# Optimization experiments

Hardware: AMD Instinct MI355X
Metric: run time of the kernel (lower is better)

Reference implementation:

```python
import jax, jax.numpy as jnp
import numpy as np

N = 50000      # nodes per graph
E = 800000     # edges per graph
F_IN = 128     # num_node_features
HID = 128      # hidden_dim
OUT = 128      # output_dim
C = 40         # num_classes
NEG_SLOPE = 0.2


def setup_inputs() -> dict:
    key = jax.random.key(0)
    ks = jax.random.split(key, 28)
    def p(k, shape, scale=0.05):
        return jax.random.normal(k, shape, jnp.float32) * scale
    inp = {
        "x": jax.random.normal(ks[0], (N, F_IN), jnp.float32),
        "y": jax.random.normal(ks[1], (N, F_IN), jnp.float32),
        "edge_index_x": jax.random.randint(ks[2], (2, E), 0, N),
        "edge_index_y": jax.random.randint(ks[3], (2, E), 0, N),
        # MultiheadAttention 1 (packed qkv in_proj like torch)
        "attn1_in_w": p(ks[4], (3 * F_IN, F_IN)),
        "attn1_in_b": p(ks[5], (3 * F_IN,)),
        "attn1_out_w": p(ks[6], (F_IN, F_IN)),
        "attn1_out_b": p(ks[7], (F_IN,)),
        # MultiheadAttention 2
        "attn2_in_w": p(ks[8], (3 * F_IN, F_IN)),
        "attn2_in_b": p(ks[9], (3 * F_IN,)),
        "attn2_out_w": p(ks[10], (F_IN, F_IN)),
        "attn2_out_b": p(ks[11], (F_IN,)),
        # gat1 (shared by x and y paths)
        "gat1_w": p(ks[12], (HID, F_IN)),
        "gat1_asrc": p(ks[13], (HID,)),
        "gat1_adst": p(ks[14], (HID,)),
        "gat1_b": p(ks[15], (HID,)),
        # gat2_x
        "gat2x_w": p(ks[16], (OUT, HID)),
        "gat2x_asrc": p(ks[17], (OUT,)),
        "gat2x_adst": p(ks[18], (OUT,)),
        "gat2x_b": p(ks[19], (OUT,)),
        # gat2_y
        "gat2y_w": p(ks[20], (OUT, HID)),
        "gat2y_asrc": p(ks[21], (OUT,)),
        "gat2y_adst": p(ks[22], (OUT,)),
        "gat2y_b": p(ks[23], (OUT,)),
        # fc
        "fc_w": p(ks[24], (C, 2 * OUT + F_IN)),
        "fc_b": p(ks[25], (C,)),
    }
    return inp


def _mha_len1(x, in_w, in_b, out_w, out_b):
    # x.unsqueeze(0) in torch -> seq_len=1 (batch=N). Softmax over a single
    # key is identically 1, so attention output == V; q/k projections cancel.
    d = x.shape[-1]
    v = x @ in_w[2 * d:].T + in_b[2 * d:]
    return v @ out_w.T + out_b


def _gat_conv(x, edge_index, W, a_src, a_dst, b):
    # PyG GATConv, heads=1, concat=True, add_self_loops=True
    n = x.shape[0]
    loop = jnp.arange(n)
    src = jnp.concatenate([edge_index[0], loop])  # message sources j
    dst = jnp.concatenate([edge_index[1], loop])  # message targets i
    h = x @ W.T                                   # [n, out]
    e = jax.nn.leaky_relu((h @ a_src)[src] + (h @ a_dst)[dst], NEG_SLOPE)
    # segment softmax over destination node neighborhoods
    m = jax.ops.segment_max(e, dst, num_segments=n)
    ex = jnp.exp(e - m[dst])
    s = jax.ops.segment_sum(ex, dst, num_segments=n)
    alpha = ex / (s[dst] + 1e-16)
    out = jax.ops.segment_sum(alpha[:, None] * h[src], dst, num_segments=n)
    return out + b


def reference(x, y, edge_index_x, edge_index_y,
              attn1_in_w, attn1_in_b, attn1_out_w, attn1_out_b,
              attn2_in_w, attn2_in_b, attn2_out_w, attn2_out_b,
              gat1_w, gat1_asrc, gat1_adst, gat1_b,
              gat2x_w, gat2x_asrc, gat2x_adst, gat2x_b,
              gat2y_w, gat2y_asrc, gat2y_adst, gat2y_b,
              fc_w, fc_b):
    x_res = x
    xa = _mha_len1(x, attn1_in_w, attn1_in_b, attn1_out_w, attn1_out_b)
    hx = jax.nn.relu(_gat_conv(xa, edge_index_x, gat1_w, gat1_asrc, gat1_adst, gat1_b))
    # dropout is a no-op in eval mode
    ox = _gat_conv(hx, edge_index_x, gat2x_w, gat2x_asrc, gat2x_adst, gat2x_b)

    ya = _mha_len1(y, attn2_in_w, attn2_in_b, attn2_out_w, attn2_out_b)
    hy = jax.nn.relu(_gat_conv(ya, edge_index_y, gat1_w, gat1_asrc, gat1_adst, gat1_b))
    oy = _gat_conv(hy, edge_index_y, gat2y_w, gat2y_asrc, gat2y_adst, gat2y_b)

    fusion = jnp.concatenate([ox, oy, x_res], axis=1)
    out = fusion @ fc_w.T + fc_b
    return jax.nn.log_softmax(out, axis=1)
```

## Files before the change

### kernel.cpp

```cpp
#include <hip/hip_runtime.h>
#include <hip/hip_bf16.h>
#include <hip/hip_fp16.h>

#define NEG_SLOPE 0.2f
#define LOG_R 10
#define RPB (1 << LOG_R)
#define EPB 4096
#define CAPB 24576

typedef __attribute__((ext_vector_type(4))) float f32x4;
typedef __attribute__((ext_vector_type(2))) float f32x2;
typedef __attribute__((ext_vector_type(8))) short s16x8;

static __device__ __forceinline__ unsigned pkbf(float a, float b) {
    unsigned ua = __float_as_uint(a);
    ua = (ua + 0x7FFFu + ((ua >> 16) & 1u)) >> 16;
    unsigned ub = __float_as_uint(b);
    ub = (ub + 0x7FFFu + ((ub >> 16) & 1u)) & 0xFFFF0000u;
    return (ua & 0xFFFFu) | ub;
}
static __device__ __forceinline__ unsigned short bf1(float a) {
    unsigned ua = __float_as_uint(a);
    return (unsigned short)((ua + 0x7FFFu + ((ua >> 16) & 1u)) >> 16);
}
static __device__ __forceinline__ float bflo(unsigned u) { return __uint_as_float(u << 16); }
static __device__ __forceinline__ float bfhi(unsigned u) { return __uint_as_float(u & 0xFFFF0000u); }

__global__ __launch_bounds__(256) void mha_combine2(
    const float* __restrict__ iw1, const float* __restrict__ ib1,
    const float* __restrict__ ow1, const float* __restrict__ ob1,
    const float* __restrict__ iw2, const float* __restrict__ ib2,
    const float* __restrict__ ow2, const float* __restrict__ ob2,
    float* __restrict__ cw1, float* __restrict__ cb1,
    float* __restrict__ cw2, float* __restrict__ cb2)
{
    int idx = blockIdx.x * blockDim.x + threadIdx.x;
    int set = idx >> 14;
    int local = idx & 16383;
    int o = local >> 7, i = local & 127;
    const float* in_w  = set ? iw2 : iw1;
    const float* in_b  = set ? ib2 : ib1;
    const float* out_w = set ? ow2 : ow1;
    const float* out_b = set ? ob2 : ob1;
    float* combW = set ? cw2 : cw1;
    float* combb = set ? cb2 : cb1;
    float a = 0.f;
    for (int k = 0; k < 128; ++k)
        a = fmaf(out_w[o * 128 + k], in_w[(256 + k) * 128 + i], a);
    combW[local] = a;
    if (i == 0) {
        float b = out_b[o];
        for (int k = 0; k < 128; ++k)
            b = fmaf(out_w[o * 128 + k], in_b[256 + k], b);
        combb[o] = b;
    }
}

template<bool ABF, bool HFP8>
__global__ __launch_bounds__(256) void gemm_mfma2(
    const void* __restrict__ A0, const void* __restrict__ A1,
    const float* __restrict__ W0, const float* __restrict__ W1,
    const float* __restrict__ bias0, const float* __restrict__ bias1,
    const float* __restrict__ as0, const float* __restrict__ ad0,
    const float* __restrict__ as1, const float* __restrict__ ad1,
    void* __restrict__ h0, void* __restrict__ h1,
    float* __restrict__ ss0, float* __restrict__ sd0,
    float* __restrict__ ss1, float* __restrict__ sd1,
    int n, int half)
{
    __shared__ unsigned xl[64 * 64];
    __shared__ unsigned wl[128 * 64];

    int b = blockIdx.x;
    const void* Ain; const float *W, *bias, *asrc, *adst;
    void* hbs; float *ssrc, *sdst;
    if (b < half) { Ain = A0; W = W0; bias = bias0; asrc = as0; adst = ad0; hbs = h0; ssrc = ss0; sdst = sd0; }
    else { b -= half; Ain = A1; W = W1; bias = bias1; asrc = as1; adst = ad1; hbs = h1; ssrc = ss1; sdst = sd1; }

    const int t = threadIdx.x;
    const int row0 = b * 64;

#pragma unroll
    for (int i = 0; i < 4; ++i) {
        int q = t + i * 256;
        int r = q >> 4, sl = q & 15;
        int gr = row0 + r; if (gr >= n) gr = n - 1;
        unsigned p0, p1, p2, p3;
        if (ABF) {
            uint4 v = ((const uint4*)Ain)[(size_t)gr * 16 + sl];
            p0 = v.x; p1 = v.y; p2 = v.z; p3 = v.w;
        } else {
            float4 a = ((const float4*)Ain)[(size_t)gr * 32 + sl * 2];
            float4 bb = ((const float4*)Ain)[(size_t)gr * 32 + sl * 2 + 1];
            p0 = pkbf(a.x, a.y); p1 = pkbf(a.z, a.w);
            p2 = pkbf(bb.x, bb.y); p3 = pkbf(bb.z, bb.w);
        }
        int dsl = sl ^ (r & 7);
        *(uint4*)&xl[r * 64 + dsl * 4] = make_uint4(p0, p1, p2, p3);
    }
#pragma unroll
    for (int i = 0; i < 8; ++i) {
        int q = t + i * 256;
        int r = q >> 4, sl = q & 15;
        float4 a = ((const float4*)W)[(size_t)r * 32 + sl * 2];
        float4 bb = ((const float4*)W)[(size_t)r * 32 + sl * 2 + 1];
        int dsl = sl ^ (r & 7);
        *(uint4*)&wl[r * 64 + dsl * 4] = make_uint4(
            pkbf(a.x, a.y), pkbf(a.z, a.w), pkbf(bb.x, bb.y), pkbf(bb.z, bb.w));
    }
    __syncthreads();

    const int l = t & 63, w = t >> 6;
    const int c = l & 15, q4 = l >> 4;
    const int rloc = w * 16 + c;
    f32x4 acc[8];
#pragma unroll
    for (int nt = 0; nt < 8; ++nt) acc[nt] = (f32x4){0.f, 0.f, 0.f, 0.f};

#pragma unroll
    for (int s = 0; s < 4; ++s) {
        int slot = (s * 4 + q4) ^ (c & 7);
        s16x8 af = *(const s16x8*)&xl[rloc * 64 + slot * 4];
#pragma unroll
        for (int nt = 0; nt < 8; ++nt) {
            int wr = nt * 16 + c;
            s16x8 bfr = *(const s16x8*)&wl[wr * 64 + slot * 4];
            acc[nt] = __builtin_amdgcn_mfma_f32_16x16x32_bf16(af, bfr, acc[nt], 0, 0, 0);
        }
    }

    float bv[8], as8[8], ad8[8];
#pragma unroll
    for (int nt = 0; nt < 8; ++nt) {
        bv[nt]  = bias ? bias[nt * 16 + c] : 0.f;
        as8[nt] = asrc ? asrc[nt * 16 + c] : 0.f;
        ad8[nt] = asrc ? adst[nt * 16 + c] : 0.f;
    }
    float ps[4] = {0.f, 0.f, 0.f, 0.f}, pd[4] = {0.f, 0.f, 0.f, 0.f};
    const int grow0 = row0 + w * 16 + q4 * 4;
#pragma unroll
    for (int nt = 0; nt < 8; ++nt) {
#pragma unroll
        for (int j = 0; j < 4; ++j) {
            float val = acc[nt][j] + bv[nt];
            if (grow0 + j < n) {
                if (HFP8) {
                    unsigned b8 = (unsigned)__builtin_amdgcn_cvt_pk_fp8_f32(val, val, 0, false);
                    ((unsigned char*)hbs)[(size_t)(grow0 + j) * 128 + nt * 16 + c] = (unsigned char)b8;
                } else {
                    ((unsigned short*)hbs)[(size_t)(grow0 + j) * 128 + nt * 16 + c] = bf1(val);
                }
            }
            ps[j] = fmaf(val, as8[nt], ps[j]);
            pd[j] = fmaf(val, ad8[nt], pd[j]);
        }
    }
    if (asrc) {
#pragma unroll
        for (int j = 0; j < 4; ++j) {
            float a = ps[j], bb = pd[j];
#pragma unroll
            for (int o = 1; o < 16; o <<= 1) {
                a += __shfl_xor(a, o);
                bb += __shfl_xor(bb, o);
            }
            if (c == 0 && grow0 + j < n) { ssrc[grow0 + j] = a; sdst[grow0 + j] = bb; }
        }
    }
}


__global__ __launch_bounds__(256) void hist_bucket2(
    const int* __restrict__ eix, const int* __restrict__ eiy, int E, int n,
    int* __restrict__ bcx, int* __restrict__ bcy, int half)
{
    __shared__ int lh[64];
    int gb = blockIdx.x;
    const int* ei = eix; int* bc = bcx;
    if (gb >= half) { gb -= half; ei = eiy; bc = bcy; }
    int t = threadIdx.x;
    int ET = E + n;
    int nbk = (n + RPB - 1) >> LOG_R;
    for (int i = t; i < nbk; i += 256) lh[i] = 0;
    __syncthreads();
    for (int e = gb * 256 + t; e < ET; e += half * 256) {
        int d = (e < E) ? ei[E + e] : (e - E);
        atomicAdd(&lh[d >> LOG_R], 1);
    }
    __syncthreads();
    if (t < nbk) atomicAdd(&bc[t], lh[t]);
}

__global__ void bscan(
    const int* __restrict__ bcx, const int* __restrict__ bcy, int nbk,
    int* __restrict__ bbx, int* __restrict__ bby,
    int* __restrict__ curx, int* __restrict__ cury,
    int* __restrict__ offx_n, int* __restrict__ offy_n)
{
    int w = threadIdx.x >> 6, lane = threadIdx.x & 63;
    if (w > 1) return;
    const int* bc = w ? bcy : bcx;
    int* bb  = w ? bby : bbx;
    int* cur = w ? cury : curx;
    int* offn = w ? offy_n : offx_n;
    int c = (lane < nbk) ? bc[lane] : 0;
    int v = c;
#pragma unroll
    for (int o = 1; o < 64; o <<= 1) {
        int u = __shfl_up(v, o);
        if (lane >= o) v += u;
    }
    int excl = v - c;
    if (lane < nbk) { bb[lane] = excl; cur[lane] = excl; }
    if (lane == 63) { bb[nbk] = v; *offn = v; }
}

__global__ __launch_bounds__(256) void bucket_pass(
    const int* __restrict__ eix, const int* __restrict__ eiy, int E, int n,
    int* __restrict__ curx, int* __restrict__ cury,
    unsigned* __restrict__ pkx, unsigned* __restrict__ pky, int half)
{
    __shared__ int lhist[64], lbase[64], gbase[64], lpos[64];
    __shared__ unsigned stg[EPB];
    __shared__ int gidx[EPB];
    int gb = blockIdx.x;
    const int* ei = eix; int* bcur = curx; unsigned* pk = pkx;
    if (gb >= half) { gb -= half; ei = eiy; bcur = cury; pk = pky; }
    const int t = threadIdx.x;
    const int ET = E + n;
    const int nbk = (n + RPB - 1) >> LOG_R;
    const int base = gb * EPB;

    for (int i = t; i < nbk; i += 256) lhist[i] = 0;
    __syncthreads();

    unsigned mypk[16];
    int myb[16];
#pragma unroll
    for (int k = 0; k < 16; ++k) {
        int e = base + k * 256 + t;
        if (e < ET) {
            int s, d;
            if (e < E) { s = ei[e]; d = ei[E + e]; }
            else       { s = e - E; d = e - E; }
            myb[k] = d >> LOG_R;
            mypk[k] = ((unsigned)s << LOG_R) | (unsigned)(d & (RPB - 1));
            atomicAdd(&lhist[myb[k]], 1);
        } else myb[k] = -1;
    }
    __syncthreads();

    if (t < 64) {
        int c = (t < nbk) ? lhist[t] : 0;
        int v = c;
#pragma unroll
        for (int o = 1; o < 64; o <<= 1) {
            int u = __shfl_up(v, o);
            if (t >= o) v += u;
        }
        int excl = v - c;
        if (t < nbk) {
            lbase[t] = excl;
            lpos[t] = excl;
            gbase[t] = c ? atomicAdd(&bcur[t], c) : 0;
        }
    }
    __syncthreads();

#pragma unroll
    for (int k = 0; k < 16; ++k) {
        if (myb[k] >= 0) {
            int p = atomicAdd(&lpos[myb[k]], 1);
            stg[p] = mypk[k];
            gidx[p] = gbase[myb[k]] + (p - lbase[myb[k]]);
        }
    }
    __syncthreads();

    int tot = lbase[nbk - 1] + lhist[nbk - 1];
    for (int i = t; i < tot; i += 256) pk[gidx[i]] = stg[i];
}

__global__ __launch_bounds__(256) void fine_sort(
    const unsigned* __restrict__ pkx, const unsigned* __restrict__ pky,
    const int* __restrict__ bbx, const int* __restrict__ bby,
    int* __restrict__ offx, int* __restrict__ offy,
    unsigned short* __restrict__ csx, unsigned short* __restrict__ csy,
    int n, int half)
{
    __shared__ int cur[RPB];
    __shared__ int ws[256];
    __shared__ unsigned short outs[CAPB];
    int gb = blockIdx.x;
    const unsigned* pk; const int* bb; int* off; unsigned short* cs;
    if (gb < half) { pk = pkx; bb = bbx; off = offx; cs = csx; }
    else { gb -= half; pk = pky; bb = bby; off = offy; cs = csy; }
    const int t = threadIdx.x;
    const int d0 = gb << LOG_R;
    const int nd = min(RPB, n - d0);
    const int base = bb[gb];
    const int sz = bb[gb + 1] - base;

    for (int i = t; i < RPB; i += 256) cur[i] = 0;
    __syncthreads();
    for (int i = t; i < sz; i += 256)
        atomicAdd(&cur[pk[base + i] & (RPB - 1)], 1);
    __syncthreads();

    int c0 = cur[t * 4], c1 = cur[t * 4 + 1], c2 = cur[t * 4 + 2], c3 = cur[t * 4 + 3];
    int s = c0 + c1 + c2 + c3;
    ws[t] = s; __syncthreads();
    for (int o = 1; o < 256; o <<= 1) {
        int a = (t >= o) ? ws[t - o] : 0;
        __syncthreads();
        ws[t] += a;
        __syncthreads();
    }
    int ex = ws[t] - s;
    int e0 = ex, e1 = ex + c0, e2 = e1 + c1, e3 = e2 + c2;
    cur[t * 4] = e0; cur[t * 4 + 1] = e1; cur[t * 4 + 2] = e2; cur[t * 4 + 3] = e3;
    int i0 = t * 4;
    if (i0     < nd) off[d0 + i0]     = base + e0;
    if (i0 + 1 < nd) off[d0 + i0 + 1] = base + e1;
    if (i0 + 2 < nd) off[d0 + i0 + 2] = base + e2;
    if (i0 + 3 < nd) off[d0 + i0 + 3] = base + e3;
    __syncthreads();

    if (sz <= CAPB) {
        for (int i = t; i < sz; i += 256) {
            unsigned p = pk[base + i];
            int pos = atomicAdd(&cur[p & (RPB - 1)], 1);
            outs[pos] = (unsigned short)(p >> LOG_R);
        }
        __syncthreads();
        for (int i = t; i < sz; i += 256) cs[base + i] = outs[i];
    } else {
        for (int i = t; i < sz; i += 256) {
            unsigned p = pk[base + i];
            int pos = atomicAdd(&cur[p & (RPB - 1)], 1);
            cs[base + pos] = (unsigned short)(p >> LOG_R);
        }
    }
}

__global__ __launch_bounds__(256) void gat_aggregate2(
    const int* __restrict__ off0, const unsigned short* __restrict__ cs0,
    const float* __restrict__ ss0, const float* __restrict__ sd0,
    const unsigned char* __restrict__ hb0, const float* __restrict__ bias0,
    unsigned* __restrict__ out0,
    const int* __restrict__ off1, const unsigned short* __restrict__ cs1,
    const float* __restrict__ ss1, const float* __restrict__ sd1,
    const unsigned char* __restrict__ hb1, const float* __restrict__ bias1,
    unsigned* __restrict__ out1,
    int n, int relu, int half)
{
    __shared__ uint2 stg[4][2][32];
    int b = blockIdx.x;
    const int *off; const unsigned short *csrc; const float *ssrc, *sdst, *bias;
    const unsigned char* hb; unsigned* outu;
    if (b < half) { off = off0; csrc = cs0; ssrc = ss0; sdst = sd0; hb = hb0; bias = bias0; outu = out0; }
    else { b -= half; off = off1; csrc = cs1; ssrc = ss1; sdst = sd1; hb = hb1; bias = bias1; outu = out1; }

    const int w = threadIdx.x >> 6;
    const int lane = threadIdx.x & 63;
    const int hw = lane >> 5;
    const int l32 = lane & 31;
    int node = b * 8 + w * 2 + hw;
    const int valid = node < n;
    if (node >= n) node = n - 1;
    const int p0 = off[node], p1 = off[node + 1];
    const int deg = p1 - p0;
    const float sd = sdst[node];

    unsigned mysrc = 0; float myv = -INFINITY;
    if (l32 < deg) {
        mysrc = csrc[p0 + l32];
        float v = ssrc[mysrc] + sd;
        myv = (v > 0.f) ? v : NEG_SLOPE * v;
    }
    float m = myv;
    for (int p = p0 + 32 + l32; p < p1; p += 32) {
        int s = csrc[p];
        float v = ssrc[s] + sd;
        v = (v > 0.f) ? v : NEG_SLOPE * v;
        m = fmaxf(m, v);
    }
#pragma unroll
    for (int o = 16; o; o >>= 1) m = fmaxf(m, __shfl_xor(m, o));

    float myex = (l32 < deg) ? __expf(myv - m) : 0.f;
    float part = myex;
    for (int p = p0 + 32 + l32; p < p1; p += 32) {
        int s = csrc[p];
        float v = ssrc[s] + sd;
        v = (v > 0.f) ? v : NEG_SLOPE * v;
        part += __expf(v - m);
    }
    float ssum = part;
#pragma unroll
    for (int o = 16; o; o >>= 1) ssum += __shfl_xor(ssum, o);

    stg[w][hw][l32] = make_uint2(mysrc, __float_as_uint(myex));

    const unsigned clo = (unsigned)l32 * 4u;
    float a0 = 0.f, a1 = 0.f, a2 = 0.f, a3 = 0.f;

    int jcap = deg < 32 ? deg : 32;
    int j = 0;
    for (; j + 8 <= jcap; j += 8) {
        uint2 q[8];
#pragma unroll
        for (int k = 0; k < 8; ++k) q[k] = stg[w][hw][j + k];
        unsigned u[8];
#pragma unroll
        for (int k = 0; k < 8; ++k)
            u[k] = *(const unsigned*)(hb + (((size_t)q[k].x << 7) | clo));
#pragma unroll
        for (int k = 0; k < 8; ++k) {
            f32x2 flo = __builtin_amdgcn_cvt_pk_f32_fp8((int)u[k], false);
            f32x2 fhi = __builtin_amdgcn_cvt_pk_f32_fp8((int)u[k], true);
            float e = __uint_as_float(q[k].y);
            a0 = fmaf(e, flo[0], a0);
            a1 = fmaf(e, flo[1], a1);
            a2 = fmaf(e, fhi[0], a2);
            a3 = fmaf(e, fhi[1], a3);
        }
    }
    for (; j < jcap; ++j) {
        uint2 q = stg[w][hw][j];
        unsigned u = *(const unsigned*)(hb + (((size_t)q.x << 7) | clo));
        f32x2 flo = __builtin_amdgcn_cvt_pk_f32_fp8((int)u, false);
        f32x2 fhi = __builtin_amdgcn_cvt_pk_f32_fp8((int)u, true);
        float e = __uint_as_float(q.y);
        a0 = fmaf(e, flo[0], a0);
        a1 = fmaf(e, flo[1], a1);
        a2 = fmaf(e, fhi[0], a2);
        a3 = fmaf(e, fhi[1], a3);
    }
    for (int p = p0 + 32; p < p1; ++p) {
        int s = csrc[p];
        float v = ssrc[s] + sd;
        v = (v > 0.f) ? v : NEG_SLOPE * v;
        float e = __expf(v - m);
        unsigned u = *(const unsigned*)(hb + (((size_t)s << 7) | clo));
        f32x2 flo = __builtin_amdgcn_cvt_pk_f32_fp8((int)u, false);
        f32x2 fhi = __builtin_amdgcn_cvt_pk_f32_fp8((int)u, true);
        a0 = fmaf(e, flo[0], a0);
        a1 = fmaf(e, flo[1], a1);
        a2 = fmaf(e, fhi[0], a2);
        a3 = fmaf(e, fhi[1], a3);
    }

    float inv = 1.f / (ssum + 1e-16f);
    float4 bv = ((const float4*)bias)[l32];
    float o0 = fmaf(a0, inv, bv.x);
    float o1 = fmaf(a1, inv, bv.y);
    float o2 = fmaf(a2, inv, bv.z);
    float o3 = fmaf(a3, inv, bv.w);
    if (relu) {
        o0 = fmaxf(o0, 0.f); o1 = fmaxf(o1, 0.f);
        o2 = fmaxf(o2, 0.f); o3 = fmaxf(o3, 0.f);
    }
    if (valid)
        ((uint2*)(outu + (size_t)node * 64))[l32] = make_uint2(pkbf(o0, o1), pkbf(o2, o3));
}

__global__ __launch_bounds__(256) void fc_logsoftmax(
    const unsigned* __restrict__ oxu, const unsigned* __restrict__ oyu,
    const float* __restrict__ xres,
    const float* __restrict__ fcw, const float* __restrict__ fcb,
    float* __restrict__ out, int n)
{
    __shared__ float wt[40 * 132];
    const int t = threadIdx.x;
    const int node0 = blockIdx.x * 128;
    const int c0 = (t & 7) * 5;
    int gr[4];
#pragma unroll
    for (int j = 0; j < 4; ++j) {
        gr[j] = node0 + (t >> 3) * 4 + j;
        if (gr[j] >= n) gr[j] = n - 1;
    }

    float acc[4][5] = {};

    for (int kc = 0; kc < 3; ++kc) {
        __syncthreads();
        for (int i = t; i < 40 * 32; i += 256) {
            int cc = i >> 5, c4 = i & 31;
            *(float4*)&wt[cc * 132 + c4 * 4] = ((const float4*)fcw)[(size_t)cc * 96 + kc * 32 + c4];
        }
        __syncthreads();
#pragma unroll 4
        for (int k4 = 0; k4 < 32; ++k4) {
            float4 xv[4];
            if (kc == 2) {
#pragma unroll
                for (int j = 0; j < 4; ++j)
                    xv[j] = ((const float4*)xres)[(size_t)gr[j] * 32 + k4];
            } else {
                const unsigned* S = kc ? oyu : oxu;
#pragma unroll
                for (int j = 0; j < 4; ++j) {
                    uint2 u = *(const uint2*)&S[(size_t)gr[j] * 64 + k4 * 2];
                    xv[j] = make_float4(bflo(u.x), bfhi(u.x), bflo(u.y), bfhi(u.y));
                }
            }
#pragma unroll
            for (int j5 = 0; j5 < 5; ++j5) {
                float4 wv = *(const float4*)&wt[(c0 + j5) * 132 + k4 * 4];
#pragma unroll
                for (int j = 0; j < 4; ++j) {
                    acc[j][j5] = fmaf(xv[j].x, wv.x, acc[j][j5]);
                    acc[j][j5] = fmaf(xv[j].y, wv.y, acc[j][j5]);
                    acc[j][j5] = fmaf(xv[j].z, wv.z, acc[j][j5]);
                    acc[j][j5] = fmaf(xv[j].w, wv.w, acc[j][j5]);
                }
            }
        }
    }

    float fb[5];
#pragma unroll
    for (int j5 = 0; j5 < 5; ++j5) fb[j5] = fcb[c0 + j5];

#pragma unroll
    for (int j = 0; j < 4; ++j) {
        float m0 = -INFINITY;
#pragma unroll
        for (int j5 = 0; j5 < 5; ++j5) { acc[j][j5] += fb[j5]; m0 = fmaxf(m0, acc[j][j5]); }
#pragma unroll
        for (int o = 1; o < 8; o <<= 1) m0 = fmaxf(m0, __shfl_xor(m0, o));
        float s0 = 0.f;
#pragma unroll
        for (int j5 = 0; j5 < 5; ++j5) s0 += __expf(acc[j][j5] - m0);
#pragma unroll
        for (int o = 1; o < 8; o <<= 1) s0 += __shfl_xor(s0, o);
        float lse = m0 + logf(s0);
#pragma unroll
        for (int j5 = 0; j5 < 5; ++j5)
            out[(size_t)gr[j] * 40 + c0 + j5] = acc[j][j5] - lse;
    }
}

extern "C" void kernel_launch(void* const* d_in, const int* in_sizes, int n_in,
                              void* d_out, int out_size, void* d_ws, size_t ws_size,
                              hipStream_t stream)
{
    const float* x    = (const float*)d_in[0];
    const float* y    = (const float*)d_in[1];
    const int*   eix  = (const int*)d_in[2];
    const int*   eiy  = (const int*)d_in[3];
    const float* a1iw = (const float*)d_in[4];
    const float* a1ib = (const float*)d_in[5];
    const float* a1ow = (const float*)d_in[6];
    const float* a1ob = (const float*)d_in[7];
    const float* a2iw = (const float*)d_in[8];
    const float* a2ib = (const float*)d_in[9];
    const float* a2ow = (const float*)d_in[10];
    const float* a2ob = (const float*)d_in[11];
    const float* g1w  = (const float*)d_in[12];
    const float* g1as = (const float*)d_in[13];
    const float* g1ad = (const float*)d_in[14];
    const float* g1b  = (const float*)d_in[15];
    const float* g2xw = (const float*)d_in[16];
    const float* g2xas= (const float*)d_in[17];
    const float* g2xad= (const float*)d_in[18];
    const float* g2xb = (const float*)d_in[19];
    const float* g2yw = (const float*)d_in[20];
    const float* g2yas= (const float*)d_in[21];
    const float* g2yad= (const float*)d_in[22];
    const float* g2yb = (const float*)d_in[23];
    const float* fcw  = (const float*)d_in[24];
    const float* fcb  = (const float*)d_in[25];
    float* outp = (float*)d_out;

    const int N = in_sizes[0] / 128;
    const int E = in_sizes[2] / 2;
    (void)n_in; (void)out_size; (void)ws_size;

    size_t NU = (size_t)N * 64;
    unsigned* u0 = (unsigned*)d_ws;
    unsigned* u1 = u0 + NU;
    unsigned* u2 = u1 + NU;
    unsigned* u3 = u2 + NU;
    float* ssx = (float*)(u3 + NU);
    float* sdx = ssx + N;
    float* ssy = sdx + N;
    float* sdy = ssy + N;
    float* cw1 = sdy + N;
    float* cb1 = cw1 + 128 * 128;
    float* cw2 = cb1 + 128;
    float* cb2 = cw2 + 128 * 128;
    const int Npad = (N + 4) & ~3;
    int* offx = (int*)(cb2 + 128);
    int* offy = offx + Npad;
    int* bbx  = offy + Npad;
    int* bby  = bbx + 128;
    int* bcx  = bby + 128;
    int* bcy  = bcx + 64;
    int* curx = bcy + 64;
    int* cury = curx + 64;
    unsigned* pkx = (unsigned*)(cury + 64);
    unsigned* pky = pkx + (E + N);
    unsigned short* csx = (unsigned short*)(pky + (E + N));
    unsigned short* csy = csx + (((E + N) + 1) & ~1);

    const int ET = E + N;
    const int NBK = (N + RPB - 1) >> LOG_R;
    const int gG = (N + 63) / 64;
    const int gA = (N + 7) / 8;
    const int nAB = (ET + EPB - 1) / EPB;

    mha_combine2<<<128, 256, 0, stream>>>(a1iw, a1ib, a1ow, a1ob,
                                          a2iw, a2ib, a2ow, a2ob,
                                          cw1, cb1, cw2, cb2);

    hipMemsetAsync(bcx, 0, 128 * sizeof(int), stream);
    hist_bucket2<<<256, 256, 0, stream>>>(eix, eiy, E, N, bcx, bcy, 128);
    bscan<<<1, 128, 0, stream>>>(bcx, bcy, NBK, bbx, bby, curx, cury, offx + N, offy + N);
    bucket_pass<<<2 * nAB, 256, 0, stream>>>(eix, eiy, E, N, curx, cury, pkx, pky, nAB);
    fine_sort<<<2 * NBK, 256, 0, stream>>>(pkx, pky, bbx, bby, offx, offy, csx, csy, N, NBK);

    gemm_mfma2<false, false><<<2 * gG, 256, 0, stream>>>(
        x, y, cw1, cw2, cb1, cb2,
        nullptr, nullptr, nullptr, nullptr,
        u0, u2,
        nullptr, nullptr, nullptr, nullptr, N, gG);

    gemm_mfma2<true, true><<<2 * gG, 256, 0, stream>>>(
        u0, u2, g1w, g1w, nullptr, nullptr,
        g1as, g1ad, g1as, g1ad,
        u1, u3,
        ssx, sdx, ssy, sdy, N, gG);
    gat_aggregate2<<<2 * gA, 256, 0, stream>>>(
        offx, csx, ssx, sdx, (const unsigned char*)u1, g1b, u0,
        offy, csy, ssy, sdy, (const unsigned char*)u3, g1b, u2,
        N, 1, gA);

    gemm_mfma2<true, true><<<2 * gG, 256, 0, stream>>>(
        u0, u2, g2xw, g2yw, nullptr, nullptr,
        g2xas, g2xad, g2yas, g2yad,
        u1, u3,
        ssx, sdx, ssy, sdy, N, gG);
    gat_aggregate2<<<2 * gA, 256, 0, stream>>>(
        offx, csx, ssx, sdx, (const unsigned char*)u1, g2xb, u0,
        offy, csy, ssy, sdy, (const unsigned char*)u3, g2yb, u2,
        N, 0, gA);

    fc_logsoftmax<<<(N + 127) / 128, 256, 0, stream>>>(u0, u2, x, fcw, fcb, outp, N);
}
```

Measured before the change: 254.6 us.

## Compute final FC layer with bf16 MFMA and pre-packed bf16 weights

Rewrites the fc+log_softmax kernel to stage 64 rows of the concatenated [ox, oy, x_res] features as bf16 in swizzled LDS and compute logits with 16x16x32 bf16 MFMA instructions. The 40 classes are padded to 48. The FC weights are converted once to padded bf16 by a new prep kernel. This replaces the scalar FP32 FMA loop to cut ALU time in the final layer. It adds one small launch and rounds x_res and the weights to bf16, which lowers accuracy.

```diff
diff --git a/kernel.cpp b/kernel.cpp
--- a/kernel.cpp
+++ b/kernel.cpp
@@ -56,6 +56,19 @@
     }
 }
 
+__global__ __launch_bounds__(256) void fcw_prep(
+    const float* __restrict__ fcw, unsigned* __restrict__ wbf)
+{
+    int i = blockIdx.x * 256 + threadIdx.x;
+    if (i >= 48 * 192) return;
+    unsigned v = 0;
+    if (i < 40 * 192) {
+        float2 f = ((const float2*)fcw)[i];
+        v = pkbf(f.x, f.y);
+    }
+    wbf[i] = v;
+}
+
 template<bool ABF, bool HFP8>
 __global__ __launch_bounds__(256) void gemm_mfma2(
     const void* __restrict__ A0, const void* __restrict__ A1,
@@ -468,78 +481,78 @@
 __global__ __launch_bounds__(256) void fc_logsoftmax(
     const unsigned* __restrict__ oxu, const unsigned* __restrict__ oyu,
     const float* __restrict__ xres,
-    const float* __restrict__ fcw, const float* __restrict__ fcb,
+    const unsigned* __restrict__ wbf, const float* __restrict__ fcb,
     float* __restrict__ out, int n)
 {
-    __shared__ float wt[40 * 132];
+    __shared__ unsigned xl[64 * 192];
     const int t = threadIdx.x;
-    const int node0 = blockIdx.x * 128;
-    const int c0 = (t & 7) * 5;
-    int gr[4];
+    const int row0 = blockIdx.x * 64;
+
+#pragma unroll
+    for (int i = 0; i < 12; ++i) {
+        int q = t + i * 256;
+        int r = q / 48, sl = q % 48;
+        int gr = row0 + r; if (gr >= n) gr = n - 1;
+        uint4 v;
+        if (sl < 16) {
+            v = ((const uint4*)oxu)[(size_t)gr * 16 + sl];
+        } else if (sl < 32) {
+            v = ((const uint4*)oyu)[(size_t)gr * 16 + (sl - 16)];
+        } else {
+            float4 a = ((const float4*)xres)[(size_t)gr * 32 + (sl - 32) * 2];
+            float4 b = ((const float4*)xres)[(size_t)gr * 32 + (sl - 32) * 2 + 1];
+            v = make_uint4(pkbf(a.x, a.y), pkbf(a.z, a.w), pkbf(b.x, b.y), pkbf(b.z, b.w));
+        }
+        int dsl = sl ^ (r & 7);
+        *(uint4*)&xl[r * 192 + dsl * 4] = v;
+    }
+    __syncthreads();
+
+    const int l = t & 63, w = t >> 6;
+    const int c = l & 15, q4 = l >> 4;
+    const int rloc = w * 16 + c;
+    f32x4 acc[3];
+#pragma unroll
+    for (int nt = 0; nt < 3; ++nt) acc[nt] = (f32x4){0.f, 0.f, 0.f, 0.f};
+
+#pragma unroll
+    for (int ks = 0; ks < 12; ++ks) {
+        int gslot = ks * 4 + q4;
+        int slot = gslot ^ (rloc & 7);
+        s16x8 af = *(const s16x8*)&xl[rloc * 192 + slot * 4];
+#pragma unroll
+        for (int nt = 0; nt < 3; ++nt) {
+            int wr = nt * 16 + c;
+            s16x8 bfr = *(const s16x8*)&wbf[(size_t)wr * 192 + gslot * 4];
+            acc[nt] = __builtin_amdgcn_mfma_f32_16x16x32_bf16(af, bfr, acc[nt], 0, 0, 0);
+        }
+    }
+
+    float vb[3];
+#pragma unroll
+    for (int nt = 0; nt < 3; ++nt) {
+        int col = nt * 16 + c;
+        vb[nt] = (col < 40) ? fcb[col] : 0.f;
+    }
+    const int grow0 = row0 + w * 16 + q4 * 4;
 #pragma unroll
     for (int j = 0; j < 4; ++j) {
-        gr[j] = node0 + (t >> 3) * 4 + j;
-        if (gr[j] >= n) gr[j] = n - 1;
-    }
-
-    float acc[4][5] = {};
-
-    for (int kc = 0; kc < 3; ++kc) {
-        __syncthreads();
-        for (int i = t; i < 40 * 32; i += 256) {
-            int cc = i >> 5, c4 = i & 31;
-            *(float4*)&wt[cc * 132 + c4 * 4] = ((const float4*)fcw)[(size_t)cc * 96 + kc * 32 + c4];
-        }
-        __syncthreads();
-#pragma unroll 4
-        for (int k4 = 0; k4 < 32; ++k4) {
-            float4 xv[4];
-            if (kc == 2) {
-#pragma unroll
-                for (int j = 0; j < 4; ++j)
-                    xv[j] = ((const float4*)xres)[(size_t)gr[j] * 32 + k4];
-            } else {
-                const unsigned* S = kc ? oyu : oxu;
-#pragma unroll
-                for (int j = 0; j < 4; ++j) {
-                    uint2 u = *(const uint2*)&S[(size_t)gr[j] * 64 + k4 * 2];
-                    xv[j] = make_float4(bflo(u.x), bfhi(u.x), bflo(u.y), bfhi(u.y));
-                }
-            }
-#pragma unroll
-            for (int j5 = 0; j5 < 5; ++j5) {
-                float4 wv = *(const float4*)&wt[(c0 + j5) * 132 + k4 * 4];
-#pragma unroll
-                for (int j = 0; j < 4; ++j) {
-                    acc[j][j5] = fmaf(xv[j].x, wv.x, acc[j][j5]);
-                    acc[j][j5] = fmaf(xv[j].y, wv.y, acc[j][j5]);
-                    acc[j][j5] = fmaf(xv[j].z, wv.z, acc[j][j5]);
-                    acc[j][j5] = fmaf(xv[j].w, wv.w, acc[j][j5]);
-                }
-            }
-        }
-    }
-
-    float fb[5];
-#pragma unroll
-    for (int j5 = 0; j5 < 5; ++j5) fb[j5] = fcb[c0 + j5];
-
-#pragma unroll
-    for (int j = 0; j < 4; ++j) {
-        float m0 = -INFINITY;
-#pragma unroll
-        for (int j5 = 0; j5 < 5; ++j5) { acc[j][j5] += fb[j5]; m0 = fmaxf(m0, acc[j][j5]); }
-#pragma unroll
-        for (int o = 1; o < 8; o <<= 1) m0 = fmaxf(m0, __shfl_xor(m0, o));
-        float s0 = 0.f;
-#pragma unroll
-        for (int j5 = 0; j5 < 5; ++j5) s0 += __expf(acc[j][j5] - m0);
-#pragma unroll
-        for (int o = 1; o < 8; o <<= 1) s0 += __shfl_xor(s0, o);
+        float v0 = acc[0][j] + vb[0];
+        float v1 = acc[1][j] + vb[1];
+        float v2 = (c < 8) ? (acc[2][j] + vb[2]) : -INFINITY;
+        float m0 = fmaxf(fmaxf(v0, v1), v2);
+#pragma unroll
+        for (int o = 1; o < 16; o <<= 1) m0 = fmaxf(m0, __shfl_xor(m0, o));
+        float s0 = __expf(v0 - m0) + __expf(v1 - m0) + ((c < 8) ? __expf(v2 - m0) : 0.f);
+#pragma unroll
+        for (int o = 1; o < 16; o <<= 1) s0 += __shfl_xor(s0, o);
         float lse = m0 + logf(s0);
-#pragma unroll
-        for (int j5 = 0; j5 < 5; ++j5)
-            out[(size_t)gr[j] * 40 + c0 + j5] = acc[j][j5] - lse;
+        int grow = grow0 + j;
+        if (grow < n) {
+            out[(size_t)grow * 40 + c] = v0 - lse;
+            out[(size_t)grow * 40 + 16 + c] = v1 - lse;
+            if (c < 8) out[(size_t)grow * 40 + 32 + c] = v2 - lse;
+        }
     }
 }
 
@@ -605,6 +618,7 @@
     unsigned* pky = pkx + (E + N);
     unsigned short* csx = (unsigned short*)(pky + (E + N));
     unsigned short* csy = csx + (((E + N) + 1) & ~1);
+    unsigned* wbf = (unsigned*)(csy + (((E + N) + 1) & ~1));
 
     const int ET = E + N;
     const int NBK = (N + RPB - 1) >> LOG_R;
@@ -615,6 +629,7 @@
     mha_combine2<<<128, 256, 0, stream>>>(a1iw, a1ib, a1ow, a1ob,
                                           a2iw, a2ib, a2ow, a2ob,
                                           cw1, cb1, cw2, cb2);
+    fcw_prep<<<(48 * 192 + 255) / 256, 256, 0, stream>>>(fcw, wbf);
 
     hipMemsetAsync(bcx, 0, 128 * sizeof(int), stream);
     hist_bucket2<<<256, 256, 0, stream>>>(eix, eiy, E, N, bcx, bcy, 128);
@@ -648,5 +663,5 @@
         offy, csy, ssy, sdy, (const unsigned char*)u3, g2yb, u2,
         N, 0, gA);
 
-    fc_logsoftmax<<<(N + 127) / 128, 256, 0, stream>>>(u0, u2, x, fcw, fcb, outp, N);
-}
+    fc_logsoftmax<<<(N + 63) / 64, 256, 0, stream>>>(u0, u2, x, wbf, fcb, outp, N);
+}
```

Result: no change. 253.3 us (-0.5%).
